# Kernel tuning notes

Measured on AMD Instinct MI355X. Metric: run time of the kernel, lower is better.

## Reference

```python
import jax, jax.numpy as jnp
import numpy as np

NEG_BIG = -9e15
ALPHA = 0.2  # LeakyReLU negative slope


def setup_inputs() -> dict:
    key = jax.random.key(0)
    k1, k2, k3, k4 = jax.random.split(key, 4)
    N, Fin, Fout = 8192, 256, 256
    input_ = jax.random.normal(k1, (N, Fin), dtype=jnp.float32)
    adj = jax.random.randint(k2, (N, N), 0, 2, dtype=jnp.int32)
    # xavier_uniform with gain=1.414
    limW = 1.414 * np.sqrt(6.0 / (Fin + Fout))
    W = jax.random.uniform(k3, (Fin, Fout), minval=-limW, maxval=limW, dtype=jnp.float32)
    lima = 1.414 * np.sqrt(6.0 / (2 * Fout + 1))
    a = jax.random.uniform(k4, (2 * Fout, 1), minval=-lima, maxval=lima, dtype=jnp.float32)
    return {"input_": input_, "adj": adj, "W": W, "a": a}


def reference(input_, adj, W, a):
    # h: [N, F]
    h = input_ @ W
    F = h.shape[1]
    # Decompose cat([h_i, h_j]) @ a into per-node projections summed by broadcast
    src = h @ a[:F, 0]   # [N]  contribution of row node i
    dst = h @ a[F:, 0]   # [N]  contribution of col node j
    e = jax.nn.leaky_relu(src[:, None] + dst[None, :], negative_slope=ALPHA)  # [N, N]
    e = jnp.where(adj > 0, e, NEG_BIG)
    attention = jax.nn.softmax(e, axis=1)
    h_prime = attention @ h  # [N, F]
    return jax.nn.relu(h_prime)  # concat=True
```

## Files before the change

### kernel.cpp

```cpp
#include <hip/hip_runtime.h>
#include <math.h>

#define NN 8192
#define FF 256
#define ALPHA 0.2f
#define SS 4
#define JSEG (NN / SS)
#define STEPS (JSEG / 32)

typedef __bf16 bf16x8 __attribute__((ext_vector_type(8)));
typedef __bf16 bf16x4 __attribute__((ext_vector_type(4)));
typedef float  f32x4  __attribute__((ext_vector_type(4)));

__device__ __forceinline__ void dma16(const void* g, void* l) {
    __builtin_amdgcn_global_load_lds((const __attribute__((address_space(1))) void*)g,
                                     (__attribute__((address_space(3))) void*)l,
                                     16, 0, 0);
}

#define VMCNT4   asm volatile("s_waitcnt vmcnt(4)" ::: "memory")
#define LGKM0    asm volatile("s_waitcnt lgkmcnt(0)" ::: "memory")
#define BARRIER  asm volatile("s_barrier" ::: "memory")
#define FENCE    asm volatile("" ::: "memory")

__global__ __launch_bounds__(256) void k0_wt(const float* __restrict__ W,
                                             __bf16* __restrict__ WT) {
    __shared__ float ts[64][65];
    const int t = threadIdx.x;
    const int k0 = blockIdx.x * 64;
    const int n0 = blockIdx.y * 64;
    #pragma unroll
    for (int r = 0; r < 4; ++r) {
        int krow = r * 16 + (t >> 4);
        int nc4 = (t & 15) * 4;
        *(float4*)&ts[krow][nc4] = *(const float4*)&W[(size_t)(k0 + krow) * FF + n0 + nc4];
    }
    __syncthreads();
    const int nloc = t >> 2;
    const int kc = (t & 3) * 16;
    union { bf16x8 v[2]; __bf16 e[16]; } hi, lo;
    #pragma unroll
    for (int u = 0; u < 16; ++u) {
        float x = ts[kc + u][nloc];
        __bf16 h1 = (__bf16)x;
        hi.e[u] = h1;
        lo.e[u] = (__bf16)(x - (float)h1);
    }
    size_t base = (size_t)(n0 + nloc) * FF + k0 + kc;
    *(bf16x8*)&WT[base] = hi.v[0];
    *(bf16x8*)&WT[base + 8] = hi.v[1];
    size_t lbase = (size_t)FF * FF + base;
    *(bf16x8*)&WT[lbase] = lo.v[0];
    *(bf16x8*)&WT[lbase + 8] = lo.v[1];
}

__global__ __launch_bounds__(256) void k1_h(const float* __restrict__ X,
                                            const __bf16* __restrict__ WT,
                                            const float* __restrict__ a,
                                            __bf16* __restrict__ hT,
                                            float* __restrict__ src,
                                            float* __restrict__ dst) {
    __shared__ __bf16 ax[2][32][40];
    __shared__ float hs[32][264];
    __shared__ float red[2][4][32];
    const int t = threadIdx.x;
    const int i0 = blockIdx.x * 32;
    const int l = t & 63, wv = t >> 6, ln = l & 15, g = l >> 4;
    f32x4 acc[2][4];
    #pragma unroll
    for (int mt = 0; mt < 2; ++mt)
        #pragma unroll
        for (int nt = 0; nt < 4; ++nt)
            acc[mt][nt] = (f32x4){0.f, 0.f, 0.f, 0.f};

    for (int ks = 0; ks < 8; ++ks) {
        const int k0 = ks * 32;
        {
            int row = t >> 3, c4 = (t & 7) * 4;
            float4 xv = *(const float4*)&X[(size_t)(i0 + row) * FF + k0 + c4];
            bf16x4 hi4, lo4;
            float xs_[4] = {xv.x, xv.y, xv.z, xv.w};
            #pragma unroll
            for (int u = 0; u < 4; ++u) {
                __bf16 h1 = (__bf16)xs_[u];
                hi4[u] = h1;
                lo4[u] = (__bf16)(xs_[u] - (float)h1);
            }
            *(bf16x4*)&ax[0][row][c4] = hi4;
            *(bf16x4*)&ax[1][row][c4] = lo4;
        }
        __syncthreads();
        bf16x8 ah[2], al[2];
        ah[0] = *(bf16x8*)&ax[0][ln][g * 8];
        ah[1] = *(bf16x8*)&ax[0][16 + ln][g * 8];
        al[0] = *(bf16x8*)&ax[1][ln][g * 8];
        al[1] = *(bf16x8*)&ax[1][16 + ln][g * 8];
        #pragma unroll
        for (int nt = 0; nt < 4; ++nt) {
            const int n = wv * 64 + nt * 16 + ln;
            bf16x8 bh8 = *(const bf16x8*)&WT[(size_t)n * FF + k0 + g * 8];
            bf16x8 bl8 = *(const bf16x8*)&WT[(size_t)(FF + n) * FF + k0 + g * 8];
            #pragma unroll
            for (int mt = 0; mt < 2; ++mt) {
                acc[mt][nt] = __builtin_amdgcn_mfma_f32_16x16x32_bf16(ah[mt], bh8, acc[mt][nt], 0, 0, 0);
                acc[mt][nt] = __builtin_amdgcn_mfma_f32_16x16x32_bf16(ah[mt], bl8, acc[mt][nt], 0, 0, 0);
                acc[mt][nt] = __builtin_amdgcn_mfma_f32_16x16x32_bf16(al[mt], bh8, acc[mt][nt], 0, 0, 0);
            }
        }
        __syncthreads();
    }
    float an[4], ad[4];
    #pragma unroll
    for (int nt = 0; nt < 4; ++nt) {
        an[nt] = a[wv * 64 + nt * 16 + ln];
        ad[nt] = a[FF + wv * 64 + nt * 16 + ln];
    }
    float sp[2][4], dp[2][4];
    #pragma unroll
    for (int mt = 0; mt < 2; ++mt)
        #pragma unroll
        for (int rg = 0; rg < 4; ++rg) { sp[mt][rg] = 0.f; dp[mt][rg] = 0.f; }
    #pragma unroll
    for (int mt = 0; mt < 2; ++mt)
        #pragma unroll
        for (int nt = 0; nt < 4; ++nt)
            #pragma unroll
            for (int rg = 0; rg < 4; ++rg) {
                float v = acc[mt][nt][rg];
                hs[mt * 16 + g * 4 + rg][wv * 64 + nt * 16 + ln] = v;
                sp[mt][rg] += v * an[nt];
                dp[mt][rg] += v * ad[nt];
            }
    #pragma unroll
    for (int mk = 1; mk < 16; mk <<= 1)
        #pragma unroll
        for (int mt = 0; mt < 2; ++mt)
            #pragma unroll
            for (int rg = 0; rg < 4; ++rg) {
                sp[mt][rg] += __shfl_xor(sp[mt][rg], mk);
                dp[mt][rg] += __shfl_xor(dp[mt][rg], mk);
            }
    if (ln == 0) {
        #pragma unroll
        for (int mt = 0; mt < 2; ++mt)
            #pragma unroll
            for (int rg = 0; rg < 4; ++rg) {
                red[0][wv][mt * 16 + g * 4 + rg] = sp[mt][rg];
                red[1][wv][mt * 16 + g * 4 + rg] = dp[mt][rg];
            }
    }
    __syncthreads();
    if (t < 32) {
        src[i0 + t] = red[0][0][t] + red[0][1][t] + red[0][2][t] + red[0][3][t];
        dst[i0 + t] = red[1][0][t] + red[1][1][t] + red[1][2][t] + red[1][3][t];
    }
    {
        const int f = t;
        #pragma unroll
        for (int jc = 0; jc < 4; ++jc) {
            union { bf16x8 v; __bf16 e[8]; } hi, lo;
            #pragma unroll
            for (int u = 0; u < 8; ++u) {
                float x = hs[jc * 8 + u][f];
                __bf16 h1 = (__bf16)x;
                hi.e[u] = h1;
                lo.e[u] = (__bf16)(x - (float)h1);
            }
            *(bf16x8*)&hT[(size_t)f * NN + i0 + jc * 8] = hi.v;
            *(bf16x8*)&hT[(size_t)(FF + f) * NN + i0 + jc * 8] = lo.v;
        }
    }
}

__global__ __launch_bounds__(256) void k2b_max(const float* __restrict__ dst,
                                               float* __restrict__ maxd) {
    __shared__ float red[256];
    float m = -1e30f;
    #pragma unroll
    for (int r = 0; r < NN / 1024; ++r) {
        float4 v = *(const float4*)&dst[(r * 256 + threadIdx.x) * 4];
        m = fmaxf(m, fmaxf(fmaxf(v.x, v.y), fmaxf(v.z, v.w)));
    }
    red[threadIdx.x] = m;
    __syncthreads();
    for (int s = 128; s > 0; s >>= 1) {
        if (threadIdx.x < s) red[threadIdx.x] = fmaxf(red[threadIdx.x], red[threadIdx.x + s]);
        __syncthreads();
    }
    if (threadIdx.x == 0) maxd[0] = red[0];
}

__global__ __launch_bounds__(256, 3) void k3_attn(const int* __restrict__ adj,
                                                  const __bf16* __restrict__ hT,
                                                  const float* __restrict__ src,
                                                  const float* __restrict__ dst,
                                                  const float* __restrict__ maxd,
                                                  float* __restrict__ num,
                                                  float* __restrict__ den) {
    __shared__ __bf16 bh[2][1024 * 8];
    const int t = threadIdx.x;
    const int l = t & 63, wv = t >> 6, ln = l & 15, g = l >> 4;
    const int it = blockIdx.x & 127;
    const int seg = blockIdx.x >> 7;
    const int i0 = it * 64;
    const int jbeg = seg * JSEG;
    const int row = i0 + wv * 16 + ln;
    const float maxdv = maxd[0];
    const float src_r = src[row];
    const float e0 = src_r + maxdv;
    const float m_r = e0 > 0.f ? e0 : ALPHA * e0;

    int ga[4], cb[4];
    #pragma unroll
    for (int r = 0; r < 4; ++r) {
        int cbase = r * 256 + wv * 64;
        int c = cbase + l;
        int f = c >> 2;
        int pc = c & 3;
        int jc = pc ^ ((f >> 1) & 3);
        ga[r] = f * NN + jc * 8;
        cb[r] = __builtin_amdgcn_readfirstlane(cbase);
    }
    const int* arow = adj + (size_t)row * NN + g * 8;
    const float* drow = dst + g * 8;

    const int rb = ln * 64 + ((g ^ ((ln >> 1) & 3)) * 16);
    const char* bh0 = (const char*)&bh[0][0] + rb;
    const char* bh1 = (const char*)&bh[1][0] + rb;

    int4 a0e, a1e, a0o, a1o;
    float4 d0e, d1e, d0o, d1o;

    a0e = *(const int4*)(arow + jbeg);
    a1e = *(const int4*)(arow + jbeg + 4);
    d0e = *(const float4*)(drow + jbeg);
    d1e = *(const float4*)(drow + jbeg + 4);
    FENCE;
    #pragma unroll
    for (int r = 0; r < 4; ++r)
        dma16(&hT[ga[r] + jbeg], &bh[0][cb[r] * 8]);
    FENCE;
    a0o = *(const int4*)(arow + jbeg + 32);
    a1o = *(const int4*)(arow + jbeg + 32 + 4);
    d0o = *(const float4*)(drow + jbeg + 32);
    d1o = *(const float4*)(drow + jbeg + 32 + 4);
    FENCE;

    float den_reg = 0.f;
    f32x4 acc[16];
    #pragma unroll
    for (int nt = 0; nt < 16; ++nt) acc[nt] = (f32x4){0.f, 0.f, 0.f, 0.f};

#define K3_WCOMP(A0_, A1_, D0_, D1_, AF_)                                     \
    {                                                                         \
        const int av[8] = {A0_.x, A0_.y, A0_.z, A0_.w,                        \
                           A1_.x, A1_.y, A1_.z, A1_.w};                       \
        const float dv[8] = {D0_.x, D0_.y, D0_.z, D0_.w,                      \
                             D1_.x, D1_.y, D1_.z, D1_.w};                     \
        _Pragma("unroll")                                                     \
        for (int u = 0; u < 8; ++u) {                                         \
            float e = src_r + dv[u];                                          \
            e = e > 0.f ? e : ALPHA * e;                                      \
            float w = (av[u] > 0) ? __expf(e - m_r) : 0.f;                    \
            den_reg += w;                                                     \
            AF_[u] = (__bf16)w;                                               \
        }                                                                     \
    }

#define K3_PREF(A0_, A1_, D0_, D1_, JN_)                                      \
    A0_ = *(const int4*)(arow + (JN_));                                       \
    A1_ = *(const int4*)(arow + (JN_) + 4);                                   \
    D0_ = *(const float4*)(drow + (JN_));                                     \
    D1_ = *(const float4*)(drow + (JN_) + 4);

#define K3_DMA(J1_, P_)                                                       \
    {                                                                         \
        _Pragma("unroll")                                                     \
        for (int r = 0; r < 4; ++r)                                           \
            dma16(&hT[ga[r] + (J1_)], &bh[P_][cb[r] * 8]);                    \
    }

#define K3_MFMA(AF_, BP_)                                                     \
    {                                                                         \
        _Pragma("unroll")                                                     \
        for (int nt = 0; nt < 16; ++nt) {                                     \
            bf16x8 bfr = *(const bf16x8*)((BP_) + nt * 1024);                 \
            acc[nt] = __builtin_amdgcn_mfma_f32_16x16x32_bf16(                \
                AF_, bfr, acc[nt], 0, 0, 0);                                  \
        }                                                                     \
    }

    for (int su = 0; su < STEPS; su += 2) {
        bf16x8 afe;
        K3_WCOMP(a0e, a1e, d0e, d1e, afe);
        {
            const int jn = (su + 2 < STEPS) ? jbeg + (su + 2) * 32 : jbeg;
            K3_PREF(a0e, a1e, d0e, d1e, jn);
        }
        FENCE; VMCNT4; LGKM0; BARRIER;
        K3_DMA(jbeg + (su + 1) * 32, 1);
        FENCE;
        K3_MFMA(afe, bh0);
        bf16x8 afo;
        K3_WCOMP(a0o, a1o, d0o, d1o, afo);
        {
            const int jn = (su + 3 < STEPS) ? jbeg + (su + 3) * 32 : jbeg;
            K3_PREF(a0o, a1o, d0o, d1o, jn);
        }
        FENCE; VMCNT4; LGKM0; BARRIER;
        {
            const int j2 = (su + 2 < STEPS) ? jbeg + (su + 2) * 32 : jbeg;
            K3_DMA(j2, 0);
        }
        FENCE;
        K3_MFMA(afo, bh1);
    }
    den_reg += __shfl_xor(den_reg, 16);
    den_reg += __shfl_xor(den_reg, 32);
    if (g == 0) den[(size_t)seg * NN + row] = den_reg;
    #pragma unroll
    for (int nt = 0; nt < 16; ++nt)
        #pragma unroll
        for (int rg = 0; rg < 4; ++rg)
            num[((size_t)seg * NN + i0 + wv * 16 + g * 4 + rg) * FF
                + nt * 16 + ln] = acc[nt][rg];
}

__global__ __launch_bounds__(256) void k4_out(const float* __restrict__ num,
                                              const float* __restrict__ den,
                                              float* __restrict__ out) {
    size_t f4 = (size_t)blockIdx.x * 256 + threadIdx.x;
    int i = (int)(f4 >> 6);
    int c4 = (int)(f4 & 63) << 2;
    float4 s = make_float4(0.f, 0.f, 0.f, 0.f);
    float d = 0.f;
    #pragma unroll
    for (int sg = 0; sg < SS; ++sg) {
        float4 v = *(const float4*)&num[((size_t)sg * NN + i) * FF + c4];
        s.x += v.x; s.y += v.y; s.z += v.z; s.w += v.w;
        d += den[(size_t)sg * NN + i];
    }
    float inv = 1.f / d;
    float4 o;
    o.x = fmaxf(s.x * inv, 0.f);
    o.y = fmaxf(s.y * inv, 0.f);
    o.z = fmaxf(s.z * inv, 0.f);
    o.w = fmaxf(s.w * inv, 0.f);
    *(float4*)&out[(size_t)i * FF + c4] = o;
}

extern "C" void kernel_launch(void* const* d_in, const int* in_sizes, int n_in,
                              void* d_out, int out_size, void* d_ws, size_t ws_size,
                              hipStream_t stream) {
    const float* X  = (const float*)d_in[0];
    const int*  adj = (const int*)d_in[1];
    const float* W  = (const float*)d_in[2];
    const float* a  = (const float*)d_in[3];
    float* out = (float*)d_out;
    char* ws = (char*)d_ws;

    const size_t off_hT   = 0;
    const size_t off_wt   = off_hT + (size_t)2 * FF * NN * 2;
    const size_t off_src  = off_wt + (size_t)2 * FF * FF * 2;
    const size_t off_dst  = off_src + (size_t)NN * 4;
    const size_t off_maxd = off_dst + (size_t)NN * 4;
    const size_t off_num  = off_maxd + 256;
    const size_t off_den  = off_num + (size_t)SS * NN * FF * 4;

    __bf16* hT_ws = (__bf16*)(ws + off_hT);
    __bf16* wt_ws = (__bf16*)(ws + off_wt);
    float* src_ws = (float*)(ws + off_src);
    float* dst_ws = (float*)(ws + off_dst);
    float* maxd   = (float*)(ws + off_maxd);
    float* num_ws = (float*)(ws + off_num);
    float* den_ws = (float*)(ws + off_den);

    k0_wt<<<dim3(FF / 64, FF / 64), 256, 0, stream>>>(W, wt_ws);
    k1_h<<<NN / 32, 256, 0, stream>>>(X, wt_ws, a, hT_ws, src_ws, dst_ws);
    k2b_max<<<1, 256, 0, stream>>>(dst_ws, maxd);
    k3_attn<<<(NN / 64) * SS, 256, 0, stream>>>(adj, hT_ws, src_ws, dst_ws, maxd,
                                                num_ws, den_ws);
    k4_out<<<(NN * FF / 4) / 256, 256, 0, stream>>>(num_ws, den_ws, out);
}
```

Measured before the change: 466.7 us.

## Pre-pack adjacency into bitmask and stage mask and dst in LDS for attention

A new streaming kernel packs the int32 adjacency matrix into a 1-bit-per-edge mask using wave shuffles. The attention kernel then loads each block's mask tile and its dst slice into LDS once, instead of issuing per-lane strided int4/float4 global loads inside the main loop. The unused low-part bf16 split of h is no longer written, which removes dead stores. The main loop is simplified to one step per iteration with a full vmcnt(0) wait. That may expose more hT DMA latency than the previous two-deep prefetch schedule.

Measured after the change: 456.2 us. 2.3% less time.

```diff
diff --git a/kernel.cpp b/kernel.cpp
--- a/kernel.cpp
+++ b/kernel.cpp
@@ -18,7 +18,7 @@
                                      16, 0, 0);
 }
 
-#define VMCNT4   asm volatile("s_waitcnt vmcnt(4)" ::: "memory")
+#define VMCNT0   asm volatile("s_waitcnt vmcnt(0)" ::: "memory")
 #define LGKM0    asm volatile("s_waitcnt lgkmcnt(0)" ::: "memory")
 #define BARRIER  asm volatile("s_barrier" ::: "memory")
 #define FENCE    asm volatile("" ::: "memory")
@@ -158,17 +158,34 @@
         const int f = t;
         #pragma unroll
         for (int jc = 0; jc < 4; ++jc) {
-            union { bf16x8 v; __bf16 e[8]; } hi, lo;
+            union { bf16x8 v; __bf16 e[8]; } hi;
             #pragma unroll
             for (int u = 0; u < 8; ++u) {
                 float x = hs[jc * 8 + u][f];
-                __bf16 h1 = (__bf16)x;
-                hi.e[u] = h1;
-                lo.e[u] = (__bf16)(x - (float)h1);
+                hi.e[u] = (__bf16)x;
             }
             *(bf16x8*)&hT[(size_t)f * NN + i0 + jc * 8] = hi.v;
-            *(bf16x8*)&hT[(size_t)(FF + f) * NN + i0 + jc * 8] = lo.v;
-        }
+        }
+    }
+}
+
+__global__ __launch_bounds__(256) void k2a_pack(const int* __restrict__ adj,
+                                                unsigned* __restrict__ bits) {
+    const size_t total4 = (size_t)NN * NN / 4;
+    const int l = threadIdx.x & 63;
+    const int base = l & 56;
+    size_t t = (size_t)blockIdx.x * 256 + threadIdx.x;
+    const size_t stride = (size_t)gridDim.x * 256;
+    for (; t < total4; t += stride) {
+        int4 v = ((const int4*)adj)[t];
+        unsigned nib = (unsigned)(v.x > 0) | ((unsigned)(v.y > 0) << 1)
+                     | ((unsigned)(v.z > 0) << 2) | ((unsigned)(v.w > 0) << 3);
+        unsigned w = 0;
+        #pragma unroll
+        for (int k = 0; k < 8; ++k)
+            w |= (unsigned)__shfl((int)nib, base + k) << (4 * k);
+        if ((l & 7) == 0)
+            bits[t >> 3] = w;
     }
 }
 
@@ -190,7 +207,7 @@
     if (threadIdx.x == 0) maxd[0] = red[0];
 }
 
-__global__ __launch_bounds__(256, 3) void k3_attn(const int* __restrict__ adj,
+__global__ __launch_bounds__(256, 3) void k3_attn(const unsigned* __restrict__ bits,
                                                   const __bf16* __restrict__ hT,
                                                   const float* __restrict__ src,
                                                   const float* __restrict__ dst,
@@ -198,17 +215,32 @@
                                                   float* __restrict__ num,
                                                   float* __restrict__ den) {
     __shared__ __bf16 bh[2][1024 * 8];
+    __shared__ unsigned mlds[64 * 68];
+    __shared__ float dsts[JSEG];
     const int t = threadIdx.x;
     const int l = t & 63, wv = t >> 6, ln = l & 15, g = l >> 4;
     const int it = blockIdx.x & 127;
     const int seg = blockIdx.x >> 7;
     const int i0 = it * 64;
     const int jbeg = seg * JSEG;
-    const int row = i0 + wv * 16 + ln;
+    const int rl = wv * 16 + ln;
+    const int row = i0 + rl;
     const float maxdv = maxd[0];
     const float src_r = src[row];
     const float e0 = src_r + maxdv;
     const float m_r = e0 > 0.f ? e0 : ALPHA * e0;
+
+    {
+        int r = t >> 2;
+        const int4* gsrc = (const int4*)(bits + (size_t)(i0 + r) * (NN / 32) + (jbeg >> 5));
+        int4* ldst = (int4*)&mlds[r * 68];
+        #pragma unroll
+        for (int u = 0; u < 4; ++u)
+            ldst[u * 4 + (t & 3)] = gsrc[u * 4 + (t & 3)];
+    }
+    #pragma unroll
+    for (int u = 0; u < 2; ++u)
+        *(float4*)&dsts[(u * 256 + t) * 4] = *(const float4*)&dst[jbeg + (u * 256 + t) * 4];
 
     int ga[4], cb[4];
     #pragma unroll
@@ -221,99 +253,53 @@
         ga[r] = f * NN + jc * 8;
         cb[r] = __builtin_amdgcn_readfirstlane(cbase);
     }
-    const int* arow = adj + (size_t)row * NN + g * 8;
-    const float* drow = dst + g * 8;
-
     const int rb = ln * 64 + ((g ^ ((ln >> 1) & 3)) * 16);
     const char* bh0 = (const char*)&bh[0][0] + rb;
     const char* bh1 = (const char*)&bh[1][0] + rb;
 
-    int4 a0e, a1e, a0o, a1o;
-    float4 d0e, d1e, d0o, d1o;
-
-    a0e = *(const int4*)(arow + jbeg);
-    a1e = *(const int4*)(arow + jbeg + 4);
-    d0e = *(const float4*)(drow + jbeg);
-    d1e = *(const float4*)(drow + jbeg + 4);
-    FENCE;
     #pragma unroll
     for (int r = 0; r < 4; ++r)
         dma16(&hT[ga[r] + jbeg], &bh[0][cb[r] * 8]);
-    FENCE;
-    a0o = *(const int4*)(arow + jbeg + 32);
-    a1o = *(const int4*)(arow + jbeg + 32 + 4);
-    d0o = *(const float4*)(drow + jbeg + 32);
-    d1o = *(const float4*)(drow + jbeg + 32 + 4);
-    FENCE;
+    __syncthreads();
 
     float den_reg = 0.f;
     f32x4 acc[16];
     #pragma unroll
     for (int nt = 0; nt < 16; ++nt) acc[nt] = (f32x4){0.f, 0.f, 0.f, 0.f};
 
-#define K3_WCOMP(A0_, A1_, D0_, D1_, AF_)                                     \
-    {                                                                         \
-        const int av[8] = {A0_.x, A0_.y, A0_.z, A0_.w,                        \
-                           A1_.x, A1_.y, A1_.z, A1_.w};                       \
-        const float dv[8] = {D0_.x, D0_.y, D0_.z, D0_.w,                      \
-                             D1_.x, D1_.y, D1_.z, D1_.w};                     \
-        _Pragma("unroll")                                                     \
-        for (int u = 0; u < 8; ++u) {                                         \
-            float e = src_r + dv[u];                                          \
-            e = e > 0.f ? e : ALPHA * e;                                      \
-            float w = (av[u] > 0) ? __expf(e - m_r) : 0.f;                    \
-            den_reg += w;                                                     \
-            AF_[u] = (__bf16)w;                                               \
-        }                                                                     \
-    }
-
-#define K3_PREF(A0_, A1_, D0_, D1_, JN_)                                      \
-    A0_ = *(const int4*)(arow + (JN_));                                       \
-    A1_ = *(const int4*)(arow + (JN_) + 4);                                   \
-    D0_ = *(const float4*)(drow + (JN_));                                     \
-    D1_ = *(const float4*)(drow + (JN_) + 4);
-
-#define K3_DMA(J1_, P_)                                                       \
-    {                                                                         \
-        _Pragma("unroll")                                                     \
-        for (int r = 0; r < 4; ++r)                                           \
-            dma16(&hT[ga[r] + (J1_)], &bh[P_][cb[r] * 8]);                    \
-    }
-
-#define K3_MFMA(AF_, BP_)                                                     \
-    {                                                                         \
-        _Pragma("unroll")                                                     \
-        for (int nt = 0; nt < 16; ++nt) {                                     \
-            bf16x8 bfr = *(const bf16x8*)((BP_) + nt * 1024);                 \
-            acc[nt] = __builtin_amdgcn_mfma_f32_16x16x32_bf16(                \
-                AF_, bfr, acc[nt], 0, 0, 0);                                  \
-        }                                                                     \
-    }
-
-    for (int su = 0; su < STEPS; su += 2) {
-        bf16x8 afe;
-        K3_WCOMP(a0e, a1e, d0e, d1e, afe);
+    for (int s = 0; s < STEPS; ++s) {
+        unsigned mb = (mlds[rl * 68 + s] >> (g * 8)) & 0xffu;
+        const float* dp = &dsts[s * 32 + g * 8];
+        float4 dq0 = *(const float4*)dp;
+        float4 dq1 = *(const float4*)(dp + 4);
+        const float dv[8] = {dq0.x, dq0.y, dq0.z, dq0.w,
+                             dq1.x, dq1.y, dq1.z, dq1.w};
+        union { bf16x8 v; __bf16 e[8]; } af;
+        #pragma unroll
+        for (int u = 0; u < 8; ++u) {
+            float e = src_r + dv[u];
+            e = e > 0.f ? e : ALPHA * e;
+            float ex = __expf(e - m_r);
+            float w = (mb & (1u << u)) ? ex : 0.f;
+            den_reg += w;
+            af.e[u] = (__bf16)w;
+        }
+        FENCE; VMCNT0; LGKM0; BARRIER;
         {
-            const int jn = (su + 2 < STEPS) ? jbeg + (su + 2) * 32 : jbeg;
-            K3_PREF(a0e, a1e, d0e, d1e, jn);
-        }
-        FENCE; VMCNT4; LGKM0; BARRIER;
-        K3_DMA(jbeg + (su + 1) * 32, 1);
+            int sn = (s + 1 < STEPS) ? s + 1 : 0;
+            int jn = jbeg + sn * 32;
+            int p = (s + 1) & 1;
+            #pragma unroll
+            for (int r = 0; r < 4; ++r)
+                dma16(&hT[ga[r] + jn], &bh[p][cb[r] * 8]);
+        }
         FENCE;
-        K3_MFMA(afe, bh0);
-        bf16x8 afo;
-        K3_WCOMP(a0o, a1o, d0o, d1o, afo);
-        {
-            const int jn = (su + 3 < STEPS) ? jbeg + (su + 3) * 32 : jbeg;
-            K3_PREF(a0o, a1o, d0o, d1o, jn);
-        }
-        FENCE; VMCNT4; LGKM0; BARRIER;
-        {
-            const int j2 = (su + 2 < STEPS) ? jbeg + (su + 2) * 32 : jbeg;
-            K3_DMA(j2, 0);
-        }
-        FENCE;
-        K3_MFMA(afo, bh1);
+        const char* bp = (s & 1) ? bh1 : bh0;
+        #pragma unroll
+        for (int nt = 0; nt < 16; ++nt) {
+            bf16x8 bfr = *(const bf16x8*)(bp + nt * 1024);
+            acc[nt] = __builtin_amdgcn_mfma_f32_16x16x32_bf16(af.v, bfr, acc[nt], 0, 0, 0);
+        }
     }
     den_reg += __shfl_xor(den_reg, 16);
     den_reg += __shfl_xor(den_reg, 32);
@@ -360,12 +346,13 @@
     char* ws = (char*)d_ws;
 
     const size_t off_hT   = 0;
-    const size_t off_wt   = off_hT + (size_t)2 * FF * NN * 2;
+    const size_t off_wt   = off_hT + (size_t)FF * NN * 2;
     const size_t off_src  = off_wt + (size_t)2 * FF * FF * 2;
     const size_t off_dst  = off_src + (size_t)NN * 4;
     const size_t off_maxd = off_dst + (size_t)NN * 4;
     const size_t off_num  = off_maxd + 256;
     const size_t off_den  = off_num + (size_t)SS * NN * FF * 4;
+    const size_t off_bits = off_den + (size_t)SS * NN * 4;
 
     __bf16* hT_ws = (__bf16*)(ws + off_hT);
     __bf16* wt_ws = (__bf16*)(ws + off_wt);
@@ -374,11 +361,13 @@
     float* maxd   = (float*)(ws + off_maxd);
     float* num_ws = (float*)(ws + off_num);
     float* den_ws = (float*)(ws + off_den);
-
+    unsigned* bits_ws = (unsigned*)(ws + off_bits);
+
+    k2a_pack<<<2048, 256, 0, stream>>>(adj, bits_ws);
     k0_wt<<<dim3(FF / 64, FF / 64), 256, 0, stream>>>(W, wt_ws);
     k1_h<<<NN / 32, 256, 0, stream>>>(X, wt_ws, a, hT_ws, src_ws, dst_ws);
     k2b_max<<<1, 256, 0, stream>>>(dst_ws, maxd);
-    k3_attn<<<(NN / 64) * SS, 256, 0, stream>>>(adj, hT_ws, src_ws, dst_ws, maxd,
+    k3_attn<<<(NN / 64) * SS, 256, 0, stream>>>(bits_ws, hT_ws, src_ws, dst_ws, maxd,
                                                 num_ws, den_ws);
     k4_out<<<(NN * FF / 4) / 256, 256, 0, stream>>>(num_ws, den_ws, out);
 }
```
